# Optimization experiments

Hardware: AMD Instinct MI355X
Metric: run time of the kernel (lower is better)

## Reference

```python
import math
import jax, jax.numpy as jnp
import numpy as np

KS = 5            # surround-modulation kernel size (create_sm_kernel default)
SIGMA_E = 1.2
SIGMA_I = 1.4
PAD = 2           # conv padding (init arg)
TOP_K = 1
T_INVERT = 1.0


def make_sm_kernel():
    # Difference-of-Gaussians kernel normalized by its center value.
    c = KS // 2
    ax = jnp.arange(KS, dtype=jnp.float32) - c
    x, y = jnp.meshgrid(ax, ax, indexing='ij')
    r2 = x ** 2 + y ** 2
    ge = jnp.exp(-r2 / (2.0 * SIGMA_E ** 2)) / (2.0 * math.pi * SIGMA_E ** 2)
    gi = jnp.exp(-r2 / (2.0 * SIGMA_I ** 2)) / (2.0 * math.pi * SIGMA_I ** 2)
    dog = ge - gi
    return dog / dog[c, c]  # [KS, KS]


def setup_inputs() -> dict:
    key = jax.random.key(0)
    k1, k2 = jax.random.split(key)
    B, Cin, H, W = 32, 32, 128, 128
    Cout, K = 64, 5
    x = jax.random.normal(k1, (B, Cin, H, W), dtype=jnp.float32)
    # weight init: weight_range * |randn|, weight_range = 25/sqrt(Cin*K*K)
    wr = 25.0 / math.sqrt(Cin * K * K)
    weight = wr * jnp.abs(jax.random.normal(k2, (Cout, Cin, K, K), dtype=jnp.float32))
    return {"x": x, "weight": weight}


def reference(x, weight):
    # symmetric padding (torch code flips edge slices -> numpy 'symmetric' mode)
    xp = jnp.pad(x, ((0, 0), (0, 0), (PAD, PAD), (PAD, PAD)), mode='symmetric')
    # main convolution (stride 1, no dilation, no bias)
    y = jax.lax.conv_general_dilated(
        xp, weight, window_strides=(1, 1), padding='VALID',
        dimension_numbers=('NCHW', 'OIHW', 'NCHW'))  # [B, Cout, H, W]
    C = y.shape[1]
    # surround modulation: depthwise conv with the fixed 5x5 DoG kernel
    sm = make_sm_kernel()
    smk = jnp.tile(sm[None, None], (C, 1, 1, 1))  # [C, 1, KS, KS]
    y = jax.lax.conv_general_dilated(
        y, smk, window_strides=(1, 1), padding='SAME',
        dimension_numbers=('NCHW', 'OIHW', 'NCHW'), feature_group_count=C)
    # soft-WTA lateral competition: softmax over channels, hard top-k mask
    s = jax.nn.softmax(T_INVERT * y, axis=1)  # [B, C, H, W]
    s_last = jnp.moveaxis(s, 1, -1)           # [B, H, W, C]
    kth = jax.lax.top_k(s_last, TOP_K)[0][..., -1]  # [B, H, W] k-th largest score
    mask = s >= kth[:, None, :, :]
    return y * mask.astype(y.dtype)
```

## Files before the change

kernel.cpp:

```cpp
#include <hip/hip_runtime.h>
#include <math.h>

#define BB   32
#define CIN  32
#define COUT 64
#define HH   128
#define WW   128
#define PLANE (HH*WW)

__device__ __forceinline__ int reflect(int p) {
    if (p < 0)   return -1 - p;
    if (p > 127) return 255 - p;
    return p;
}

__global__ __launch_bounds__(256) void repack_w(const float* __restrict__ w,
                                                float* __restrict__ wpk) {
    int i = blockIdx.x * 256 + threadIdx.x;
    if (i >= COUT * CIN * 25) return;
    int co = i / (CIN * 25);
    int rm = i - co * (CIN * 25);
    wpk[rm * COUT + co] = w[i];
}

__global__ __launch_bounds__(256) void conv_main(const float* __restrict__ x,
                                                 const float* __restrict__ wpk,
                                                 float* __restrict__ y1) {
    __shared__ float Xs[8][12][68];
    const int tid  = threadIdx.x;
    const int lane = tid & 63;
    const int wv   = tid >> 6;
    const int tile = blockIdx.x;
    const int h0   = (tile >> 1) * 8;
    const int w0   = (tile & 1) * 64;
    const int cob  = blockIdx.y * 16;
    const int b    = blockIdx.z;

    float acc[2][16];
#pragma unroll
    for (int r = 0; r < 2; ++r)
#pragma unroll
        for (int c = 0; c < 16; ++c) acc[r][c] = 0.f;

    const float* xb = x + (size_t)b * CIN * PLANE;

    for (int cc = 0; cc < CIN; cc += 8) {
        __syncthreads();
        for (int e = tid; e < 8 * 12 * 68; e += 256) {
            int ci  = e / (12 * 68);
            int rm  = e - ci * (12 * 68);
            int r   = rm / 68;
            int col = rm - r * 68;
            int sh  = reflect(h0 - 2 + r);
            int sw  = reflect(w0 - 2 + col);
            Xs[ci][r][col] = xb[(size_t)(cc + ci) * PLANE + sh * WW + sw];
        }
        __syncthreads();
#pragma unroll 1
        for (int ci = 0; ci < 8; ++ci) {
            const int cin = cc + ci;
#pragma unroll
            for (int kh = 0; kh < 5; ++kh) {
                const int r0 = 2 * wv + kh;
                float x0[5], x1[5];
#pragma unroll
                for (int kw = 0; kw < 5; ++kw) {
                    x0[kw] = Xs[ci][r0][lane + kw];
                    x1[kw] = Xs[ci][r0 + 1][lane + kw];
                }
                const float* wr = wpk + (size_t)((cin * 5 + kh) * 5) * COUT + cob;
#pragma unroll
                for (int kw = 0; kw < 5; ++kw) {
#pragma unroll
                    for (int c = 0; c < 16; ++c) {
                        float wt = wr[kw * COUT + c];
                        acc[0][c] = fmaf(x0[kw], wt, acc[0][c]);
                        acc[1][c] = fmaf(x1[kw], wt, acc[1][c]);
                    }
                }
            }
        }
    }

    float* yb = y1 + (size_t)b * COUT * PLANE;
#pragma unroll
    for (int r = 0; r < 2; ++r) {
        int hh = h0 + 2 * wv + r;
#pragma unroll
        for (int c = 0; c < 16; ++c)
            yb[(size_t)(cob + c) * PLANE + hh * WW + (w0 + lane)] = acc[r][c];
    }
}

__global__ __launch_bounds__(256) void conv_dog(const float* __restrict__ y1,
                                                float* __restrict__ y2) {
    __shared__ float T[20][132];
    __shared__ float dogk[25];
    const int tid = threadIdx.x;
    if (tid < 25) {
        int i = tid / 5, j = tid % 5;
        double dx = i - 2, dy = j - 2;
        double r2 = dx * dx + dy * dy;
        const double se2 = 2.0 * 1.2 * 1.2, si2 = 2.0 * 1.4 * 1.4;
        const double tp  = 6.283185307179586476925;
        double ge = exp(-r2 / se2) / (tp * 0.5 * se2);
        double gi = exp(-r2 / si2) / (tp * 0.5 * si2);
        double c0 = 1.0 / (tp * 0.5 * se2) - 1.0 / (tp * 0.5 * si2);
        dogk[tid] = (float)((ge - gi) / c0);
    }
    const int bc = blockIdx.y;
    const int h0 = blockIdx.x * 16;
    const float* p = y1 + (size_t)bc * PLANE;
    for (int e = tid; e < 20 * 132; e += 256) {
        int r = e / 132, c = e - (e / 132) * 132;
        int sh = h0 - 2 + r, sw = c - 2;
        float v = 0.f;
        if (sh >= 0 && sh < HH && sw >= 0 && sw < WW) v = p[sh * WW + sw];
        T[r][c] = v;
    }
    __syncthreads();
    const int col = tid & 127;
    const int rr  = tid >> 7;
    float* q = y2 + (size_t)bc * PLANE;
    for (int r8 = 0; r8 < 8; ++r8) {
        int r = rr * 8 + r8;
        float s = 0.f;
#pragma unroll
        for (int kh = 0; kh < 5; ++kh)
#pragma unroll
            for (int kw = 0; kw < 5; ++kw)
                s = fmaf(T[r + kh][col + kw], dogk[kh * 5 + kw], s);
        q[(h0 + r) * WW + col] = s;
    }
}

__global__ __launch_bounds__(256) void wta_mask(float* __restrict__ y) {
    int p   = blockIdx.x * 256 + threadIdx.x;
    int b   = p >> 14;
    int rem = p & 16383;
    float* base = y + (size_t)b * COUT * PLANE + rem;
    float v[COUT];
    float m = -INFINITY;
#pragma unroll
    for (int c = 0; c < COUT; ++c) {
        v[c] = base[(size_t)c * PLANE];
        m = fmaxf(m, v[c]);
    }
#pragma unroll
    for (int c = 0; c < COUT; ++c)
        base[(size_t)c * PLANE] = (v[c] >= m) ? v[c] : 0.f;
}

extern "C" void kernel_launch(void* const* d_in, const int* in_sizes, int n_in,
                              void* d_out, int out_size, void* d_ws, size_t ws_size,
                              hipStream_t stream) {
    const float* x = (const float*)d_in[0];
    const float* w = (const float*)d_in[1];
    float* out = (float*)d_out;

    float* y1  = (float*)d_ws;
    float* wpk = (float*)((char*)d_ws + (size_t)BB * COUT * PLANE * 4);

    repack_w<<<(COUT * CIN * 25 + 255) / 256, 256, 0, stream>>>(w, wpk);
    conv_main<<<dim3(32, 4, BB), 256, 0, stream>>>(x, wpk, y1);
    conv_dog<<<dim3(8, BB * COUT), 256, 0, stream>>>(y1, out);
    wta_mask<<<(BB * PLANE) / 256, 256, 0, stream>>>(out);
}
```

Before: 868.9 us.

## Fuse DoG conv with WTA mask and enlarge conv_main register tile

The depthwise DoG convolution and winner-take-all mask now run in one kernel. It keeps all 64 channel values per pixel in registers, so the intermediate DoG output is never written to and reread from global memory. conv_main now computes 4 output rows per wave instead of 2, with a sliding register window over input rows. This halves how often the weights are reloaded per output and reuses the shared-memory rows. The costs are more register pressure in both kernels (acc[4][16] plus xr, and v[64]) and far fewer blocks for the fused kernel (64x32), which may reduce occupancy and latency hiding.

```diff
diff --git a/kernel.cpp b/kernel.cpp
--- a/kernel.cpp
+++ b/kernel.cpp
@@ -23,50 +23,56 @@
     wpk[rm * COUT + co] = w[i];
 }
 
+#define CI_C 4
 __global__ __launch_bounds__(256) void conv_main(const float* __restrict__ x,
                                                  const float* __restrict__ wpk,
                                                  float* __restrict__ y1) {
-    __shared__ float Xs[8][12][68];
+    __shared__ float Xs[CI_C][20][68];
     const int tid  = threadIdx.x;
     const int lane = tid & 63;
     const int wv   = tid >> 6;
     const int tile = blockIdx.x;
-    const int h0   = (tile >> 1) * 8;
+    const int h0   = (tile >> 1) * 16;
     const int w0   = (tile & 1) * 64;
     const int cob  = blockIdx.y * 16;
     const int b    = blockIdx.z;
 
-    float acc[2][16];
+    float acc[4][16];
 #pragma unroll
-    for (int r = 0; r < 2; ++r)
+    for (int r = 0; r < 4; ++r)
 #pragma unroll
         for (int c = 0; c < 16; ++c) acc[r][c] = 0.f;
 
     const float* xb = x + (size_t)b * CIN * PLANE;
 
-    for (int cc = 0; cc < CIN; cc += 8) {
+    for (int cc = 0; cc < CIN; cc += CI_C) {
         __syncthreads();
-        for (int e = tid; e < 8 * 12 * 68; e += 256) {
-            int ci  = e / (12 * 68);
-            int rm  = e - ci * (12 * 68);
-            int r   = rm / 68;
-            int col = rm - r * 68;
-            int sh  = reflect(h0 - 2 + r);
-            int sw  = reflect(w0 - 2 + col);
-            Xs[ci][r][col] = xb[(size_t)(cc + ci) * PLANE + sh * WW + sw];
+        for (int ci = 0; ci < CI_C; ++ci) {
+            const float* xc = xb + (size_t)(cc + ci) * PLANE;
+            for (int e = tid; e < 20 * 68; e += 256) {
+                int r   = e / 68;
+                int col = e - r * 68;
+                int sh  = reflect(h0 - 2 + r);
+                int sw  = reflect(w0 - 2 + col);
+                Xs[ci][r][col] = xc[sh * WW + sw];
+            }
         }
         __syncthreads();
 #pragma unroll 1
-        for (int ci = 0; ci < 8; ++ci) {
+        for (int ci = 0; ci < CI_C; ++ci) {
             const int cin = cc + ci;
+            float xr[8][5];
+#pragma unroll
+            for (int q = 0; q < 4; ++q)
+#pragma unroll
+                for (int kw = 0; kw < 5; ++kw)
+                    xr[q][kw] = Xs[ci][4 * wv + q][lane + kw];
 #pragma unroll
             for (int kh = 0; kh < 5; ++kh) {
-                const int r0 = 2 * wv + kh;
-                float x0[5], x1[5];
+                if (kh > 0) {
 #pragma unroll
-                for (int kw = 0; kw < 5; ++kw) {
-                    x0[kw] = Xs[ci][r0][lane + kw];
-                    x1[kw] = Xs[ci][r0 + 1][lane + kw];
+                    for (int kw = 0; kw < 5; ++kw)
+                        xr[kh + 3][kw] = Xs[ci][4 * wv + kh + 3][lane + kw];
                 }
                 const float* wr = wpk + (size_t)((cin * 5 + kh) * 5) * COUT + cob;
 #pragma unroll
@@ -74,81 +80,84 @@
 #pragma unroll
                     for (int c = 0; c < 16; ++c) {
                         float wt = wr[kw * COUT + c];
-                        acc[0][c] = fmaf(x0[kw], wt, acc[0][c]);
-                        acc[1][c] = fmaf(x1[kw], wt, acc[1][c]);
+#pragma unroll
+                        for (int rr = 0; rr < 4; ++rr)
+                            acc[rr][c] = fmaf(xr[rr + kh][kw], wt, acc[rr][c]);
                     }
                 }
             }
         }
     }
 
-    float* yb = y1 + (size_t)b * COUT * PLANE;
+    float* yb = y1 + ((size_t)b * COUT + cob) * PLANE;
 #pragma unroll
-    for (int r = 0; r < 2; ++r) {
-        int hh = h0 + 2 * wv + r;
+    for (int rr = 0; rr < 4; ++rr) {
+        int hh = h0 + 4 * wv + rr;
 #pragma unroll
         for (int c = 0; c < 16; ++c)
-            yb[(size_t)(cob + c) * PLANE + hh * WW + (w0 + lane)] = acc[r][c];
+            yb[(size_t)c * PLANE + hh * WW + (w0 + lane)] = acc[rr][c];
     }
 }
 
-__global__ __launch_bounds__(256) void conv_dog(const float* __restrict__ y1,
-                                                float* __restrict__ y2) {
-    __shared__ float T[20][132];
-    __shared__ float dogk[25];
+__global__ __launch_bounds__(256) void dog_wta(const float* __restrict__ y1,
+                                               float* __restrict__ out) {
+    __shared__ float Ys[8][8][68];
+    __shared__ float dk[25];
     const int tid = threadIdx.x;
     if (tid < 25) {
         int i = tid / 5, j = tid % 5;
         double dx = i - 2, dy = j - 2;
         double r2 = dx * dx + dy * dy;
         const double se2 = 2.0 * 1.2 * 1.2, si2 = 2.0 * 1.4 * 1.4;
-        const double tp  = 6.283185307179586476925;
-        double ge = exp(-r2 / se2) / (tp * 0.5 * se2);
-        double gi = exp(-r2 / si2) / (tp * 0.5 * si2);
-        double c0 = 1.0 / (tp * 0.5 * se2) - 1.0 / (tp * 0.5 * si2);
-        dogk[tid] = (float)((ge - gi) / c0);
+        const double pi2 = 3.14159265358979323846 * 2.0;
+        double ge = exp(-r2 / se2) / (pi2 * 0.5 * se2);
+        double gi = exp(-r2 / si2) / (pi2 * 0.5 * si2);
+        double c0 = 1.0 / (pi2 * 0.5 * se2) - 1.0 / (pi2 * 0.5 * si2);
+        dk[tid] = (float)((ge - gi) / c0);
     }
-    const int bc = blockIdx.y;
-    const int h0 = blockIdx.x * 16;
-    const float* p = y1 + (size_t)bc * PLANE;
-    for (int e = tid; e < 20 * 132; e += 256) {
-        int r = e / 132, c = e - (e / 132) * 132;
-        int sh = h0 - 2 + r, sw = c - 2;
-        float v = 0.f;
-        if (sh >= 0 && sh < HH && sw >= 0 && sw < WW) v = p[sh * WW + sw];
-        T[r][c] = v;
+    const int col = tid & 63;
+    const int rr  = tid >> 6;
+    const int h0  = (blockIdx.x >> 1) * 4;
+    const int w0  = (blockIdx.x & 1) * 64;
+    const int b   = blockIdx.y;
+    const float* yb = y1 + (size_t)b * COUT * PLANE;
+
+    float v[COUT];
+#pragma unroll
+    for (int c8 = 0; c8 < COUT; c8 += 8) {
+        __syncthreads();
+        for (int e = tid; e < 8 * 8 * 68; e += 256) {
+            int ci = e / 544;
+            int rm = e - ci * 544;
+            int r  = rm / 68;
+            int cl = rm - r * 68;
+            int sh = h0 - 2 + r, sw = w0 - 2 + cl;
+            float val = 0.f;
+            if ((unsigned)sh < HH && (unsigned)sw < WW)
+                val = yb[(size_t)(c8 + ci) * PLANE + sh * WW + sw];
+            Ys[ci][r][cl] = val;
+        }
+        __syncthreads();
+#pragma unroll
+        for (int ci = 0; ci < 8; ++ci) {
+            float s = 0.f;
+#pragma unroll
+            for (int kh = 0; kh < 5; ++kh)
+#pragma unroll
+                for (int kw = 0; kw < 5; ++kw)
+                    s = fmaf(Ys[ci][rr + kh][col + kw], dk[kh * 5 + kw], s);
+            v[c8 + ci] = s;
+        }
     }
-    __syncthreads();
-    const int col = tid & 127;
-    const int rr  = tid >> 7;
-    float* q = y2 + (size_t)bc * PLANE;
-    for (int r8 = 0; r8 < 8; ++r8) {
-        int r = rr * 8 + r8;
-        float s = 0.f;
-#pragma unroll
-        for (int kh = 0; kh < 5; ++kh)
-#pragma unroll
-            for (int kw = 0; kw < 5; ++kw)
-                s = fmaf(T[r + kh][col + kw], dogk[kh * 5 + kw], s);
-        q[(h0 + r) * WW + col] = s;
-    }
-}
 
-__global__ __launch_bounds__(256) void wta_mask(float* __restrict__ y) {
-    int p   = blockIdx.x * 256 + threadIdx.x;
-    int b   = p >> 14;
-    int rem = p & 16383;
-    float* base = y + (size_t)b * COUT * PLANE + rem;
-    float v[COUT];
     float m = -INFINITY;
 #pragma unroll
-    for (int c = 0; c < COUT; ++c) {
-        v[c] = base[(size_t)c * PLANE];
-        m = fmaxf(m, v[c]);
-    }
+    for (int c = 0; c < COUT; ++c) m = fmaxf(m, v[c]);
+
+    float* ob = out + (size_t)b * COUT * PLANE + (h0 + rr) * WW + (w0 + col);
 #pragma unroll
     for (int c = 0; c < COUT; ++c)
-        base[(size_t)c * PLANE] = (v[c] >= m) ? v[c] : 0.f;
+        ob[(size_t)c * PLANE] = (v[c] >= m) ? v[c] : 0.f;
 }
 
 extern "C" void kernel_launch(void* const* d_in, const int* in_sizes, int n_in,
@@ -162,7 +171,6 @@
     float* wpk = (float*)((char*)d_ws + (size_t)BB * COUT * PLANE * 4);
 
     repack_w<<<(COUT * CIN * 25 + 255) / 256, 256, 0, stream>>>(w, wpk);
-    conv_main<<<dim3(32, 4, BB), 256, 0, stream>>>(x, wpk, y1);
-    conv_dog<<<dim3(8, BB * COUT), 256, 0, stream>>>(y1, out);
-    wta_mask<<<(BB * PLANE) / 256, 256, 0, stream>>>(out);
+    conv_main<<<dim3(16, 4, BB), 256, 0, stream>>>(x, wpk, y1);
+    dog_wta<<<dim3(64, BB), 256, 0, stream>>>(y1, out);
 }
```

Result: slower. 3.202 ms (+268.5%).
